# Performance work log

Hardware: AMD Instinct MI355X
Metric: run time of the kernel (lower is better)

The kernel has to match this reference:

```python
import math
import jax, jax.numpy as jnp
import numpy as np

B, CIN, COUT, K, Z, H, W = 8, 512, 512, 3, 512, 64, 64


def setup_inputs() -> dict:
    key = jax.random.key(0)
    k1, k2, k3, k4 = jax.random.split(key, 4)
    inp = {
        "input": jax.random.normal(k1, (B, CIN, H, W), dtype=jnp.float32),
        "style": jax.random.normal(k2, (B, Z), dtype=jnp.float32),
        # base conv weight: [1, out, in, k, k]
        "weight": jax.random.normal(k3, (1, COUT, CIN, K, K), dtype=jnp.float32),
        # EqualLinear modulation params (lr_mul=1, bias_init=1)
        "mod_w": jax.random.normal(k4, (CIN, Z), dtype=jnp.float32),
        "mod_b": jnp.ones((CIN,), dtype=jnp.float32),
    }
    return inp


def reference(input, style, weight, mod_w, mod_b):
    # EqualLinear: scale = 1/sqrt(z_dim), lr_mul = 1, no activation
    z_dim = mod_w.shape[1]
    mod_scale = 1.0 / math.sqrt(z_dim)
    s = style @ (mod_w * mod_scale).T + mod_b  # [B, in]

    # modulated per-sample weights: scale * base_weight * style
    in_ch, k = weight.shape[2], weight.shape[-1]
    conv_scale = 1.0 / math.sqrt(in_ch * k * k)
    w = conv_scale * weight * s[:, None, :, None, None]  # [B, out, in, k, k]

    pad = k // 2

    def conv_one(x, wb):  # x: [in, H, W], wb: [out, in, k, k]
        return jax.lax.conv_general_dilated(
            x[None], wb, window_strides=(1, 1),
            padding=[(pad, pad), (pad, pad)],
            dimension_numbers=("NCHW", "OIHW", "NCHW"),
        )[0]

    out = jax.vmap(conv_one)(input, w)  # [B, out, H, W]
    return out
```

## Files before the change

### kernel.cpp

```cpp
#include <hip/hip_runtime.h>
#include <hip/hip_bf16.h>

#define BB   8
#define CIN  512
#define COUT 512
#define ZD   512
#define HH   64
#define WW   64

#define MOD_SCALE  0.04419417382415922f
#define CONV_SCALE 0.014731391274719742f

typedef __bf16 bf16x8 __attribute__((ext_vector_type(8)));
typedef float  f32x4  __attribute__((ext_vector_type(4)));

static __device__ __forceinline__ unsigned short f32_to_bf16_rne(float f) {
    unsigned int u = __float_as_uint(f);
    u = (u + 0x7FFFu + ((u >> 16) & 1u)) >> 16;
    return (unsigned short)u;
}

__global__ void k_style(const float* __restrict__ style, const float* __restrict__ mod_w,
                        const float* __restrict__ mod_b, float* __restrict__ sconv) {
    int wid  = blockIdx.x * 4 + (threadIdx.x >> 6);
    int lane = threadIdx.x & 63;
    int b = wid >> 9;
    int i = wid & 511;
    const float4* st = (const float4*)(style + (size_t)b * ZD);
    const float4* mw = (const float4*)(mod_w + (size_t)i * ZD);
    float4 a0 = st[lane],      b0 = mw[lane];
    float4 a1 = st[lane + 64], b1 = mw[lane + 64];
    float sum = a0.x*b0.x + a0.y*b0.y + a0.z*b0.z + a0.w*b0.w
              + a1.x*b1.x + a1.y*b1.y + a1.z*b1.z + a1.w*b1.w;
    #pragma unroll
    for (int off = 32; off > 0; off >>= 1) sum += __shfl_down(sum, off);
    if (lane == 0) sconv[wid] = (sum * MOD_SCALE + mod_b[i]) * CONV_SCALE;
}

__global__ void k_zero_border(unsigned short* __restrict__ xs2p) {
    int b = blockIdx.y;
    int p = blockIdx.x * 4 + (threadIdx.x >> 6);
    int lane = threadIdx.x & 63;
    int h, w;
    if (p < 66)       { h = 0;       w = p; }
    else if (p < 132) { h = 65;      w = p - 66; }
    else if (p < 196) { h = p - 131; w = 0; }
    else              { h = p - 195; w = 65; }
    int4 z = {0, 0, 0, 0};
    *(int4*)&xs2p[((size_t)(b * 66 + h) * 66 + w) * 512 + lane * 8] = z;
}

__global__ void k_scale_input(const float* __restrict__ input, const float* __restrict__ sconv,
                              unsigned short* __restrict__ xs2p) {
    int i0 = blockIdx.x * 32;
    int h  = blockIdx.y;
    int b  = blockIdx.z;
    __shared__ unsigned short lds[64][40];
    #pragma unroll
    for (int r = 0; r < 8; ++r) {
        int ii = r * 4 + (threadIdx.x >> 6);
        int w  = threadIdx.x & 63;
        float v = input[(((size_t)b * CIN + i0 + ii) * HH + h) * WW + w];
        float s = sconv[b * CIN + i0 + ii];
        lds[w][ii] = f32_to_bf16_rne(v * s);
    }
    __syncthreads();
    int w = threadIdx.x >> 2, q = threadIdx.x & 3;
    int4 val = *(const int4*)&lds[w][q * 8];
    *(int4*)&xs2p[((size_t)(b * 66 + h + 1) * 66 + (w + 1)) * 512 + i0 + q * 8] = val;
}

__global__ void k_weight(const float* __restrict__ weight, unsigned short* __restrict__ w2g) {
    int t = blockIdx.x * 256 + threadIdx.x;
    int o = t >> 9, i = t & 511;
    int c = i >> 5, g = (i >> 3) & 3, il = i & 7;
    const float* src = weight + ((size_t)o * CIN + i) * 9;
    #pragma unroll
    for (int p = 0; p < 9; ++p) {
        size_t gran = ((size_t)(p * 16 + c) * 4 + g) * 512 + o;
        w2g[gran * 8 + il] = f32_to_bf16_rne(src[p]);
    }
}

#define WBOFF(j) ((j) * 16384)
#define XBOFF(j) (65536 + (j) * 32768)

#define GLD(srcp, ldsbyte)                                                        \
    __builtin_amdgcn_global_load_lds(                                             \
        (const __attribute__((address_space(1))) unsigned int*)(srcp),            \
        (__attribute__((address_space(3))) unsigned int*)(smb + (ldsbyte)),       \
        16, 0, 0)

__global__ __launch_bounds__(512, 2)
void k_conv(const unsigned short* __restrict__ xs2p, const unsigned short* __restrict__ w2g,
            float* __restrict__ out) {
    __shared__ unsigned short smem[65536];
    char* smb = (char*)smem;

    const int tid  = threadIdx.x;
    const int wid  = tid >> 6, lane = tid & 63;
    const int wm   = wid >> 2, wr   = wid & 3;
    const int lm   = lane & 15, hi  = lane >> 4;
    const int oc0  = blockIdx.x * 256;
    const int y0   = blockIdx.y * 4;
    const int b    = blockIdx.z;

    const int p_lin = wid * 64 + lane;
    const int xrow  = p_lin / 66;
    const int xcol  = p_lin - xrow * 66;
    const char* srcX = (const char*)xs2p;
    if (p_lin < 396)
        srcX += ((size_t)(b * 66 + y0 + xrow) * 66 + xcol) * 1024;

    const int g0   = p_lin >> 8;
    const int oc_l = p_lin & 255;
    const char* pW = (const char*)w2g + ((size_t)g0 * 512 + oc0 + oc_l) * 16;

    const int wdst = wid * 1024 + (lane & 63) * 16;

    #pragma unroll
    for (int k = 0; k < 4; ++k)
        GLD(srcX + k * 16, XBOFF(0) + k * 8192 + wdst);
    GLD(pW,                    WBOFF(0) + wdst);
    GLD(pW + 16384,            WBOFF(0) + 8192 + wdst);
    GLD(pW + 524288,           WBOFF(1) + wdst);
    GLD(pW + 524288 + 16384,   WBOFF(1) + 8192 + wdst);
    pW += 2 * 524288;
    asm volatile("s_waitcnt vmcnt(0)" ::: "memory");
    __builtin_amdgcn_s_barrier();

    f32x4 acc[8][4];
    #pragma unroll
    for (int mt = 0; mt < 8; ++mt)
        #pragma unroll
        for (int nt = 0; nt < 4; ++nt)
            acc[mt][nt] = (f32x4){0.f, 0.f, 0.f, 0.f};

    const int aoff = hi * 4096 + (wm * 128 + lm) * 16;
    const int boff = hi * 8192 + (wr * 66 + lm) * 16;

    int tap = 0, c = 0, tap2 = 2;
    bf16x8 afr[4], bfr[4];

    for (int ts = 0; ts < 144; ++ts) {
        const int wsel  = ts & 3;
        const int wsel2 = (ts + 2) & 3;
        const bool haveW2 = (ts <= 141);
        const int kh = tap / 3;
        const int kw = tap - kh * 3;
        const int ko = (kh * 66 + kw) * 16;

        const char* wbase = smb + WBOFF(wsel) + aoff;
        const char* xbase = smb + XBOFF(c & 1) + boff + ko;

        if (haveW2) GLD(pW, WBOFF(wsel2) + wdst);
        if (tap == 0 && c < 15) {
            const char* sx = srcX + (c + 1) * 64;
            #pragma unroll
            for (int k = 0; k < 4; ++k)
                GLD(sx + k * 16, XBOFF((c + 1) & 1) + k * 8192 + wdst);
        }
        #pragma unroll
        for (int mt = 0; mt < 4; ++mt) afr[mt] = *(const bf16x8*)(wbase + mt * 256);
        #pragma unroll
        for (int nt = 0; nt < 4; ++nt) bfr[nt] = *(const bf16x8*)(xbase + nt * 256);
        __builtin_amdgcn_s_barrier();
        __builtin_amdgcn_s_setprio(1);
        #pragma unroll
        for (int mt = 0; mt < 4; ++mt)
            #pragma unroll
            for (int nt = 0; nt < 4; ++nt)
                acc[mt][nt] = __builtin_amdgcn_mfma_f32_16x16x32_bf16(
                    afr[mt], bfr[nt], acc[mt][nt], 0, 0, 0);
        __builtin_amdgcn_s_setprio(0);
        __builtin_amdgcn_s_barrier();

        if (haveW2) GLD(pW + 16384, WBOFF(wsel2) + 8192 + wdst);
        #pragma unroll
        for (int mt = 0; mt < 4; ++mt) afr[mt] = *(const bf16x8*)(wbase + 1024 + mt * 256);
        __builtin_amdgcn_s_barrier();
        __builtin_amdgcn_s_setprio(1);
        #pragma unroll
        for (int mt = 0; mt < 4; ++mt)
            #pragma unroll
            for (int nt = 0; nt < 4; ++nt)
                acc[4 + mt][nt] = __builtin_amdgcn_mfma_f32_16x16x32_bf16(
                    afr[mt], bfr[nt], acc[4 + mt][nt], 0, 0, 0);
        __builtin_amdgcn_s_setprio(0);
        if (tap == 0 && c < 15)  { asm volatile("s_waitcnt vmcnt(6)" ::: "memory"); }
        else if (ts <= 141)      { asm volatile("s_waitcnt vmcnt(2)" ::: "memory"); }
        else                     { asm volatile("s_waitcnt vmcnt(0)" ::: "memory"); }
        __builtin_amdgcn_s_barrier();

        if (haveW2) {
            ++tap2;
            if (tap2 == 9) { tap2 = 0; pW -= 127 * 32768; }
            else           { pW += 524288; }
        }
        ++tap;
        if (tap == 9) { tap = 0; ++c; }
    }

    const int ybase = (y0 + wr) * 64;
    #pragma unroll
    for (int mt = 0; mt < 8; ++mt)
        #pragma unroll
        for (int nt = 0; nt < 4; ++nt)
            #pragma unroll
            for (int r = 0; r < 4; ++r) {
                int oc = oc0 + wm * 128 + mt * 16 + hi * 4 + r;
                out[((size_t)(b * COUT + oc) << 12) + ybase + nt * 16 + lm] = acc[mt][nt][r];
            }
}

extern "C" void kernel_launch(void* const* d_in, const int* in_sizes, int n_in,
                              void* d_out, int out_size, void* d_ws, size_t ws_size,
                              hipStream_t stream) {
    const float* input  = (const float*)d_in[0];
    const float* style  = (const float*)d_in[1];
    const float* weight = (const float*)d_in[2];
    const float* mod_w  = (const float*)d_in[3];
    const float* mod_b  = (const float*)d_in[4];
    float* out = (float*)d_out;

    const size_t xs2p_bytes = (size_t)BB * 66 * 66 * 512 * 2;
    const size_t w2_bytes   = (size_t)9 * 16 * 4 * 512 * 8 * 2;
    const size_t need = 16384 + xs2p_bytes + w2_bytes;
    if (ws_size < need) return;

    float*          sconv = (float*)d_ws;
    unsigned short* xs2p  = (unsigned short*)((char*)d_ws + 16384);
    unsigned short* w2g   = (unsigned short*)((char*)d_ws + 16384 + xs2p_bytes);

    hipLaunchKernelGGL(k_style,       dim3(1024),      dim3(256), 0, stream, style, mod_w, mod_b, sconv);
    hipLaunchKernelGGL(k_weight,      dim3(1024),      dim3(256), 0, stream, weight, w2g);
    hipLaunchKernelGGL(k_zero_border, dim3(65, 8),     dim3(256), 0, stream, xs2p);
    hipLaunchKernelGGL(k_scale_input, dim3(16, 64, 8), dim3(256), 0, stream, input, sconv, xs2p);
    hipLaunchKernelGGL(k_conv,        dim3(2, 16, 8),  dim3(512), 0, stream, xs2p, w2g, out);
}
```

Baseline: 181.0 us.

## Reorder weight layout contiguously per K-step and deepen weight prefetch to three stages

The weight repack now stores each (channel chunk, tap, output half) slice as one contiguous 16 KB block, so the conv kernel streams weights with a simple pointer increment. The tap loop is fully unrolled through a macro with compile-time waitcnt values. Weight prefetch moves from two buffers ahead to three of four LDS slots, and input-chunk prefetch is split across the first two taps. The aim is to cut address arithmetic and branching, improve DRAM locality of the weight stream, and hide more load latency. The cost is larger code size and hand-tuned vmcnt counts that must exactly match the issued loads.

```diff
diff --git a/kernel.cpp b/kernel.cpp
--- a/kernel.cpp
+++ b/kernel.cpp
@@ -70,20 +70,18 @@
     *(int4*)&xs2p[((size_t)(b * 66 + h + 1) * 66 + (w + 1)) * 512 + i0 + q * 8] = val;
 }
 
-__global__ void k_weight(const float* __restrict__ weight, unsigned short* __restrict__ w2g) {
+__global__ void k_weight(const float* __restrict__ weight, unsigned short* __restrict__ w3) {
     int t = blockIdx.x * 256 + threadIdx.x;
     int o = t >> 9, i = t & 511;
     int c = i >> 5, g = (i >> 3) & 3, il = i & 7;
+    int h = o >> 8, ol = o & 255;
     const float* src = weight + ((size_t)o * CIN + i) * 9;
     #pragma unroll
     for (int p = 0; p < 9; ++p) {
-        size_t gran = ((size_t)(p * 16 + c) * 4 + g) * 512 + o;
-        w2g[gran * 8 + il] = f32_to_bf16_rne(src[p]);
-    }
-}
-
-#define WBOFF(j) ((j) * 16384)
-#define XBOFF(j) (65536 + (j) * 32768)
+        size_t gran = ((size_t)(c * 9 + p) * 2 + h) * 1024 + g * 256 + ol;
+        w3[gran * 8 + il] = f32_to_bf16_rne(src[p]);
+    }
+}
 
 #define GLD(srcp, ldsbyte)                                                        \
     __builtin_amdgcn_global_load_lds(                                             \
@@ -91,8 +89,49 @@
         (__attribute__((address_space(3))) unsigned int*)(smb + (ldsbyte)),       \
         16, 0, 0)
 
+#define TAP(T, VMA, DOX, DOW) {                                                   \
+    const int ko_ = ((T) / 3) * (66 * 16) + ((T) % 3) * 16;                       \
+    const int wwr_ = (wrd + 49152) & 65535;                                       \
+    if (DOW) GLD(pW, wwr_ + wdst);                                                \
+    if ((DOX) && (T) == 0) GLD(sxn +  0, xwr + 0 * 8192 + wdst);                  \
+    if ((DOX) && (T) == 1) GLD(sxn + 32, xwr + 2 * 8192 + wdst);                  \
+    {   const char* wb = smb + wrd + aoff;                                        \
+        const char* xb = smb + xrd + boff + ko_;                                  \
+        _Pragma("unroll") for (int mt = 0; mt < 4; ++mt)                          \
+            afr[mt] = *(const bf16x8*)(wb + mt * 256);                            \
+        _Pragma("unroll") for (int nt = 0; nt < 4; ++nt)                          \
+            bfr[nt] = *(const bf16x8*)(xb + nt * 256);                            \
+    }                                                                             \
+    __builtin_amdgcn_s_barrier();                                                 \
+    __builtin_amdgcn_s_setprio(1);                                                \
+    _Pragma("unroll") for (int mt = 0; mt < 4; ++mt)                              \
+        _Pragma("unroll") for (int nt = 0; nt < 4; ++nt)                          \
+            acc[mt][nt] = __builtin_amdgcn_mfma_f32_16x16x32_bf16(                \
+                afr[mt], bfr[nt], acc[mt][nt], 0, 0, 0);                          \
+    __builtin_amdgcn_s_setprio(0);                                                \
+    __builtin_amdgcn_s_barrier();                                                 \
+    if (DOW) GLD(pW + 8192, wwr_ + 8192 + wdst);                                  \
+    if ((DOX) && (T) == 0) GLD(sxn + 16, xwr + 1 * 8192 + wdst);                  \
+    if ((DOX) && (T) == 1) GLD(sxn + 48, xwr + 3 * 8192 + wdst);                  \
+    {   const char* wb = smb + wrd + aoff + 1024;                                 \
+        _Pragma("unroll") for (int mt = 0; mt < 4; ++mt)                          \
+            afr[mt] = *(const bf16x8*)(wb + mt * 256);                            \
+    }                                                                             \
+    __builtin_amdgcn_s_barrier();                                                 \
+    __builtin_amdgcn_s_setprio(1);                                                \
+    _Pragma("unroll") for (int mt = 0; mt < 4; ++mt)                              \
+        _Pragma("unroll") for (int nt = 0; nt < 4; ++nt)                          \
+            acc[4 + mt][nt] = __builtin_amdgcn_mfma_f32_16x16x32_bf16(            \
+                afr[mt], bfr[nt], acc[4 + mt][nt], 0, 0, 0);                      \
+    __builtin_amdgcn_s_setprio(0);                                                \
+    asm volatile("s_waitcnt vmcnt(" #VMA ")" ::: "memory");                       \
+    __builtin_amdgcn_s_barrier();                                                 \
+    wrd = (wrd + 16384) & 65535;                                                  \
+    if (DOW) pW += 32768;                                                         \
+}
+
 __global__ __launch_bounds__(512, 2)
-void k_conv(const unsigned short* __restrict__ xs2p, const unsigned short* __restrict__ w2g,
+void k_conv(const unsigned short* __restrict__ xs2p, const unsigned short* __restrict__ w3,
             float* __restrict__ out) {
     __shared__ unsigned short smem[65536];
     char* smb = (char*)smem;
@@ -101,7 +140,8 @@
     const int wid  = tid >> 6, lane = tid & 63;
     const int wm   = wid >> 2, wr   = wid & 3;
     const int lm   = lane & 15, hi  = lane >> 4;
-    const int oc0  = blockIdx.x * 256;
+    const int half = blockIdx.x;
+    const int oc0  = half * 256;
     const int y0   = blockIdx.y * 4;
     const int b    = blockIdx.z;
 
@@ -112,21 +152,21 @@
     if (p_lin < 396)
         srcX += ((size_t)(b * 66 + y0 + xrow) * 66 + xcol) * 1024;
 
-    const int g0   = p_lin >> 8;
-    const int oc_l = p_lin & 255;
-    const char* pW = (const char*)w2g + ((size_t)g0 * 512 + oc0 + oc_l) * 16;
-
-    const int wdst = wid * 1024 + (lane & 63) * 16;
-
-    #pragma unroll
-    for (int k = 0; k < 4; ++k)
-        GLD(srcX + k * 16, XBOFF(0) + k * 8192 + wdst);
-    GLD(pW,                    WBOFF(0) + wdst);
-    GLD(pW + 16384,            WBOFF(0) + 8192 + wdst);
-    GLD(pW + 524288,           WBOFF(1) + wdst);
-    GLD(pW + 524288 + 16384,   WBOFF(1) + 8192 + wdst);
-    pW += 2 * 524288;
-    asm volatile("s_waitcnt vmcnt(0)" ::: "memory");
+    const char* pW0 = (const char*)w3 + (size_t)half * 16384 + p_lin * 16;
+    const int wdst = p_lin * 16;
+
+    GLD(srcX +  0, 65536 + 0 * 8192 + wdst);
+    GLD(srcX + 16, 65536 + 1 * 8192 + wdst);
+    GLD(srcX + 32, 65536 + 2 * 8192 + wdst);
+    GLD(srcX + 48, 65536 + 3 * 8192 + wdst);
+    GLD(pW0,          0     + wdst);
+    GLD(pW0 +  8192,  8192  + wdst);
+    GLD(pW0 + 32768,  16384 + wdst);
+    GLD(pW0 + 40960,  24576 + wdst);
+    GLD(pW0 + 65536,  32768 + wdst);
+    GLD(pW0 + 73728,  40960 + wdst);
+    const char* pW = pW0 + 3 * 32768;
+    asm volatile("s_waitcnt vmcnt(4)" ::: "memory");
     __builtin_amdgcn_s_barrier();
 
     f32x4 acc[8][4];
@@ -139,66 +179,23 @@
     const int aoff = hi * 4096 + (wm * 128 + lm) * 16;
     const int boff = hi * 8192 + (wr * 66 + lm) * 16;
 
-    int tap = 0, c = 0, tap2 = 2;
     bf16x8 afr[4], bfr[4];
-
-    for (int ts = 0; ts < 144; ++ts) {
-        const int wsel  = ts & 3;
-        const int wsel2 = (ts + 2) & 3;
-        const bool haveW2 = (ts <= 141);
-        const int kh = tap / 3;
-        const int kw = tap - kh * 3;
-        const int ko = (kh * 66 + kw) * 16;
-
-        const char* wbase = smb + WBOFF(wsel) + aoff;
-        const char* xbase = smb + XBOFF(c & 1) + boff + ko;
-
-        if (haveW2) GLD(pW, WBOFF(wsel2) + wdst);
-        if (tap == 0 && c < 15) {
-            const char* sx = srcX + (c + 1) * 64;
-            #pragma unroll
-            for (int k = 0; k < 4; ++k)
-                GLD(sx + k * 16, XBOFF((c + 1) & 1) + k * 8192 + wdst);
-        }
-        #pragma unroll
-        for (int mt = 0; mt < 4; ++mt) afr[mt] = *(const bf16x8*)(wbase + mt * 256);
-        #pragma unroll
-        for (int nt = 0; nt < 4; ++nt) bfr[nt] = *(const bf16x8*)(xbase + nt * 256);
-        __builtin_amdgcn_s_barrier();
-        __builtin_amdgcn_s_setprio(1);
-        #pragma unroll
-        for (int mt = 0; mt < 4; ++mt)
-            #pragma unroll
-            for (int nt = 0; nt < 4; ++nt)
-                acc[mt][nt] = __builtin_amdgcn_mfma_f32_16x16x32_bf16(
-                    afr[mt], bfr[nt], acc[mt][nt], 0, 0, 0);
-        __builtin_amdgcn_s_setprio(0);
-        __builtin_amdgcn_s_barrier();
-
-        if (haveW2) GLD(pW + 16384, WBOFF(wsel2) + 8192 + wdst);
-        #pragma unroll
-        for (int mt = 0; mt < 4; ++mt) afr[mt] = *(const bf16x8*)(wbase + 1024 + mt * 256);
-        __builtin_amdgcn_s_barrier();
-        __builtin_amdgcn_s_setprio(1);
-        #pragma unroll
-        for (int mt = 0; mt < 4; ++mt)
-            #pragma unroll
-            for (int nt = 0; nt < 4; ++nt)
-                acc[4 + mt][nt] = __builtin_amdgcn_mfma_f32_16x16x32_bf16(
-                    afr[mt], bfr[nt], acc[4 + mt][nt], 0, 0, 0);
-        __builtin_amdgcn_s_setprio(0);
-        if (tap == 0 && c < 15)  { asm volatile("s_waitcnt vmcnt(6)" ::: "memory"); }
-        else if (ts <= 141)      { asm volatile("s_waitcnt vmcnt(2)" ::: "memory"); }
-        else                     { asm volatile("s_waitcnt vmcnt(0)" ::: "memory"); }
-        __builtin_amdgcn_s_barrier();
-
-        if (haveW2) {
-            ++tap2;
-            if (tap2 == 9) { tap2 = 0; pW -= 127 * 32768; }
-            else           { pW += 524288; }
-        }
-        ++tap;
-        if (tap == 9) { tap = 0; ++c; }
+    int wrd = 0;
+    int xrd = 65536;
+    const char* sxn = srcX + 64;
+
+    for (int c = 0; c < 15; ++c) {
+        const int xwr = xrd ^ 32768;
+        TAP(0, 6, 1, 1) TAP(1, 8, 1, 1) TAP(2, 7, 0, 1) TAP(3, 5, 0, 1)
+        TAP(4, 4, 0, 1) TAP(5, 4, 0, 1) TAP(6, 4, 0, 1) TAP(7, 4, 0, 1)
+        TAP(8, 4, 0, 1)
+        sxn += 64; xrd ^= 32768;
+    }
+    {
+        const int xwr = 0; (void)xwr;
+        TAP(0, 4, 0, 1) TAP(1, 4, 0, 1) TAP(2, 4, 0, 1) TAP(3, 4, 0, 1)
+        TAP(4, 4, 0, 1) TAP(5, 4, 0, 1) TAP(6, 2, 0, 0) TAP(7, 0, 0, 0)
+        TAP(8, 0, 0, 0)
     }
 
     const int ybase = (y0 + wr) * 64;
@@ -224,17 +221,17 @@
     float* out = (float*)d_out;
 
     const size_t xs2p_bytes = (size_t)BB * 66 * 66 * 512 * 2;
-    const size_t w2_bytes   = (size_t)9 * 16 * 4 * 512 * 8 * 2;
-    const size_t need = 16384 + xs2p_bytes + w2_bytes;
+    const size_t w3_bytes   = (size_t)144 * 2 * 1024 * 8 * 2;
+    const size_t need = 16384 + xs2p_bytes + w3_bytes;
     if (ws_size < need) return;
 
     float*          sconv = (float*)d_ws;
     unsigned short* xs2p  = (unsigned short*)((char*)d_ws + 16384);
-    unsigned short* w2g   = (unsigned short*)((char*)d_ws + 16384 + xs2p_bytes);
+    unsigned short* w3    = (unsigned short*)((char*)d_ws + 16384 + xs2p_bytes);
 
     hipLaunchKernelGGL(k_style,       dim3(1024),      dim3(256), 0, stream, style, mod_w, mod_b, sconv);
-    hipLaunchKernelGGL(k_weight,      dim3(1024),      dim3(256), 0, stream, weight, w2g);
+    hipLaunchKernelGGL(k_weight,      dim3(1024),      dim3(256), 0, stream, weight, w3);
     hipLaunchKernelGGL(k_zero_border, dim3(65, 8),     dim3(256), 0, stream, xs2p);
     hipLaunchKernelGGL(k_scale_input, dim3(16, 64, 8), dim3(256), 0, stream, input, sconv, xs2p);
-    hipLaunchKernelGGL(k_conv,        dim3(2, 16, 8),  dim3(512), 0, stream, xs2p, w2g, out);
-}
+    hipLaunchKernelGGL(k_conv,        dim3(2, 16, 8),  dim3(512), 0, stream, xs2p, w3, out);
+}
```

Result: faster. 157.3 us (-13.1%).
